# Kernel optimization log

Hardware: AMD Instinct MI355X
Metric: run time of the kernel (lower is better)

## Reference

```python
import jax, jax.numpy as jnp
import numpy as np

B, T, N, F = 32, 64, 128, 128
U, K1, K2 = 64, 64, 32
EPS = 1e-3  # keras BatchNormalization default epsilon
SLOPE = 0.01  # LeakyReLU negative_slope


def setup_inputs() -> dict:
    key = jax.random.key(0)
    ks = jax.random.split(key, 16)
    g = lambda k, sh, s=0.05: jax.random.normal(k, sh, dtype=jnp.float32) * s
    inp = {
        "x": jax.random.normal(ks[0], (B, T, F), dtype=jnp.float32),
        "a": jax.random.uniform(ks[1], (B, N, N), dtype=jnp.float32),
        # LSTM (keras gate order i, f, c, o)
        "lstm_k": g(ks[2], (F, 4 * U)),
        "lstm_r": g(ks[3], (U, 4 * U)),
        "lstm_b": jnp.zeros((4 * U,), jnp.float32),
        # BatchNorm params (inference form: gamma, beta, moving mean, moving var)
        "bnl_g": jnp.ones((U,), jnp.float32), "bnl_b": jnp.zeros((U,), jnp.float32),
        "bnl_m": jnp.zeros((U,), jnp.float32), "bnl_v": jnp.ones((U,), jnp.float32),
        "w1": g(ks[4], (U, K1)), "b1": jnp.zeros((K1,), jnp.float32),
        "bn1_g": jnp.ones((K1,), jnp.float32), "bn1_b": jnp.zeros((K1,), jnp.float32),
        "bn1_m": jnp.zeros((K1,), jnp.float32), "bn1_v": jnp.ones((K1,), jnp.float32),
        "w2": g(ks[5], (K1, K2)), "b2": jnp.zeros((K2,), jnp.float32),
        "bn2_g": jnp.ones((K2,), jnp.float32), "bn2_b": jnp.zeros((K2,), jnp.float32),
        "bn2_m": jnp.zeros((K2,), jnp.float32), "bn2_v": jnp.ones((K2,), jnp.float32),
        "d1_w": g(ks[6], (T * N * K2, 3), 0.01), "d1_b": jnp.zeros((3,), jnp.float32),
        "d2_w": g(ks[7], (3, N)), "d2_b": jnp.zeros((N,), jnp.float32),
    }
    return inp


def _bn(x, g, b, m, v):
    return (x - m) * (g * jax.lax.rsqrt(v + EPS)) + b


def _leaky(x):
    return jnp.where(x >= 0, x, SLOPE * x)


def _lstm(x, Wk, Wr, b):
    # x: [B, T, F] -> hs: [B, T, U]
    xz = jnp.einsum('btf,fg->btg', x, Wk) + b  # precompute input projections
    u = Wr.shape[0]
    h0 = jnp.zeros((x.shape[0], u), x.dtype)
    c0 = jnp.zeros((x.shape[0], u), x.dtype)

    def step(carry, zt):
        h, c = carry
        z = zt + h @ Wr
        i, f, g_, o = jnp.split(z, 4, axis=-1)
        i = jax.nn.sigmoid(i); f = jax.nn.sigmoid(f)
        g_ = jnp.tanh(g_); o = jax.nn.sigmoid(o)
        c = f * c + i * g_
        h = o * jnp.tanh(c)
        return (h, c), h

    _, hs = jax.lax.scan(step, (h0, c0), xz.transpose(1, 0, 2))
    return hs.transpose(1, 0, 2)


def reference(x, a, lstm_k, lstm_r, lstm_b, bnl_g, bnl_b, bnl_m, bnl_v,
              w1, b1, bn1_g, bn1_b, bn1_m, bn1_v,
              w2, b2, bn2_g, bn2_b, bn2_m, bn2_v,
              d1_w, d1_b, d2_w, d2_b):
    h = _lstm(x, lstm_k, lstm_r, lstm_b)              # [B, T, U]
    h = _bn(h, bnl_g, bnl_b, bnl_m, bnl_v)            # inference BN; dropout is identity
    # tile each timestep's LSTM output over the N nodes, then GCN1
    support1 = jnp.einsum('btu,uk->btk', h, w1)       # [B, T, K1] (identical across nodes)
    sup1 = jnp.broadcast_to(support1[:, :, None, :], (h.shape[0], h.shape[1], N, w1.shape[1]))
    g1 = jnp.einsum('bij,btjk->btik', a, sup1) + b1   # adjacency matmul
    g1 = _leaky(g1)
    g1 = _bn(g1, bn1_g, bn1_b, bn1_m, bn1_v)
    # GCN2
    sup2 = jnp.einsum('btnk,km->btnm', g1, w2)
    g2 = jnp.einsum('bij,btjm->btim', a, sup2) + b2
    g2 = _leaky(g2)
    g2 = _bn(g2, bn2_g, bn2_b, bn2_m, bn2_v)          # [B, T, N, K2]
    flat = g2.reshape(g2.shape[0], -1)                # [B, T*N*K2]
    d1 = jax.nn.relu(flat @ d1_w + d1_b)              # [B, 3]
    return d1 @ d2_w + d2_b                           # [B, N]
```

## Files before the change

kernel.cpp:

```cpp
#include <hip/hip_runtime.h>

#define BB 32
#define TT 64
#define NN 128
#define FF 128
#define UU 64
#define K1 64
#define K2 32
#define G4 256
#define EPSV 1e-3f
#define SLOPE 0.01f

#define ALD 136
#define SLD 136
#define WLD 72

typedef __attribute__((ext_vector_type(8))) short short8;
typedef __attribute__((ext_vector_type(4))) float f32x4;

__device__ __forceinline__ float sigmoidf_(float x) {
  return __builtin_amdgcn_rcpf(1.f + __expf(-x));
}
__device__ __forceinline__ float tanhf_(float x) {
  return 1.f - 2.f * __builtin_amdgcn_rcpf(__expf(2.f * x) + 1.f);
}
__device__ __forceinline__ float leaky_(float x) { return x >= 0.f ? x : SLOPE * x; }
__device__ __forceinline__ unsigned short f2bf(float x) {
  union { float f; unsigned u; } v; v.f = x;
  unsigned r = v.u + 0x7fff + ((v.u >> 16) & 1);
  return (unsigned short)(r >> 16);
}

__global__ __launch_bounds__(256) void k_pre(const float* __restrict__ x,
                                             const float* __restrict__ wk,
                                             const float* __restrict__ bias,
                                             const float* __restrict__ a,
                                             const float* __restrict__ w2,
                                             float* __restrict__ xz,
                                             float* __restrict__ rsum,
                                             unsigned short* __restrict__ apad,
                                             unsigned short* __restrict__ w2t) {
  int tid = threadIdx.x;
  if (blockIdx.x < 32) {
    int b = blockIdx.x;
    int wave = tid >> 6, lane = tid & 63;
    const float* ab = a + (size_t)b * NN * NN;
    for (int r = 0; r < 32; ++r) {
      int row = wave * 32 + r;
      float2 v = *(const float2*)(ab + (size_t)row * NN + lane * 2);
      float s = v.x + v.y;
#pragma unroll
      for (int off = 32; off >= 1; off >>= 1) s += __shfl_down(s, off);
      if (lane == 0) rsum[b * NN + row] = s;
    }
    unsigned short* ap = apad + (size_t)b * NN * ALD;
    for (int idx = tid; idx < NN * NN; idx += 256) {
      int i = idx >> 7, j = idx & 127;
      ap[i * ALD + j] = f2bf(ab[idx]);
    }
    if (b == 0) {
      for (int idx = tid; idx < K1 * K2; idx += 256) {
        int k = idx >> 5, m = idx & 31;
        w2t[m * WLD + k] = f2bf(w2[idx]);
      }
    }
  } else {
    __shared__ float xs[8][FF];
    int row0 = (blockIdx.x - 32) * 8;
    for (int i = tid; i < 8 * FF; i += 256) xs[i >> 7][i & 127] = x[(size_t)row0 * FF + i];
    __syncthreads();
    int g = tid;
    float acc[8];
    float bg = bias[g];
#pragma unroll
    for (int r = 0; r < 8; ++r) acc[r] = bg;
    for (int f = 0; f < FF; ++f) {
      float w = wk[f * G4 + g];
#pragma unroll
      for (int r = 0; r < 8; ++r) acc[r] += xs[r][f] * w;
    }
#pragma unroll
    for (int r = 0; r < 8; ++r) xz[(size_t)(row0 + r) * G4 + g] = acc[r];
  }
}

__global__ __launch_bounds__(256, 1) void k_lstm(const float* __restrict__ xz,
                                                 const float* __restrict__ wr,
                                                 const float* __restrict__ bnl_g,
                                                 const float* __restrict__ bnl_b,
                                                 const float* __restrict__ bnl_m,
                                                 const float* __restrict__ bnl_v,
                                                 float* __restrict__ hbn) {
  __shared__ __align__(16) float hsh[2][UU];
  __shared__ __align__(16) float hist[TT][UU];
  int tid = threadIdx.x;
  int wave = tid >> 6;
  int lane = tid & 63;
  int q = lane >> 4, up = lane & 15;
  int u = wave * 16 + up;
  int g = q * 64 + u;
  int b = blockIdx.x;

  float wcol[UU];
#pragma unroll
  for (int v = 0; v < UU; ++v) wcol[v] = wr[v * G4 + g];

  float bscale = bnl_g[u] * rsqrtf(bnl_v[u] + EPSV);
  float boff = bnl_b[u] - bnl_m[u] * bscale;

  if (tid < UU) hsh[0][tid] = 0.f;

  const float* xzb = xz + (size_t)b * TT * G4;
  float cur = xzb[g];
  float c = 0.f;

  for (int t = 0; t < TT; ++t) {
    __syncthreads();
    float nxt = (t + 1 < TT) ? xzb[(t + 1) * G4 + g] : 0.f;
    const float4* h4 = (const float4*)hsh[t & 1];
    float acc0 = cur, acc1 = 0.f, acc2 = 0.f, acc3 = 0.f;
#pragma unroll
    for (int p = 0; p < 16; p += 4) {
      float4 v0 = h4[p], v1 = h4[p + 1], v2 = h4[p + 2], v3 = h4[p + 3];
      acc0 += v0.x * wcol[4 * p + 0] + v0.y * wcol[4 * p + 1] + v0.z * wcol[4 * p + 2] + v0.w * wcol[4 * p + 3];
      acc1 += v1.x * wcol[4 * p + 4] + v1.y * wcol[4 * p + 5] + v1.z * wcol[4 * p + 6] + v1.w * wcol[4 * p + 7];
      acc2 += v2.x * wcol[4 * p + 8] + v2.y * wcol[4 * p + 9] + v2.z * wcol[4 * p + 10] + v2.w * wcol[4 * p + 11];
      acc3 += v3.x * wcol[4 * p + 12] + v3.y * wcol[4 * p + 13] + v3.z * wcol[4 * p + 14] + v3.w * wcol[4 * p + 15];
    }
    float z = (acc0 + acc1) + (acc2 + acc3);
    float zi = __shfl(z, up);
    float zf = __shfl(z, up + 16);
    float zg = __shfl(z, up + 32);
    float zo = __shfl(z, up + 48);
    float i_ = sigmoidf_(zi), f_ = sigmoidf_(zf), g_ = tanhf_(zg), o_ = sigmoidf_(zo);
    c = f_ * c + i_ * g_;
    float h = o_ * tanhf_(c);
    if (q == 0) {
      hsh[(t & 1) ^ 1][u] = h;
      hist[t][u] = h * bscale + boff;
    }
    cur = nxt;
  }
  __syncthreads();
  const float4* hs4 = (const float4*)&hist[0][0];
  float4* hb4 = (float4*)(hbn + (size_t)b * TT * UU);
#pragma unroll
  for (int k = 0; k < 4; ++k) hb4[tid + k * 256] = hs4[tid + k * 256];
}

__global__ __launch_bounds__(256) void k_gcn(
    const float* __restrict__ hbn, const float* __restrict__ w1,
    const float* __restrict__ rsum,
    const unsigned short* __restrict__ apad, const unsigned short* __restrict__ w2t,
    const float* __restrict__ b1,
    const float* __restrict__ bn1_g, const float* __restrict__ bn1_b,
    const float* __restrict__ bn1_m, const float* __restrict__ bn1_v,
    const float* __restrict__ b2,
    const float* __restrict__ bn2_g, const float* __restrict__ bn2_b,
    const float* __restrict__ bn2_m, const float* __restrict__ bn2_v,
    const float* __restrict__ d1w, float* __restrict__ part) {
  __shared__ unsigned short a_lds[NN * ALD];
  __shared__ unsigned short s2_lds[K2 * SLD];
  __shared__ unsigned short w2_lds[K2 * WLD];
  __shared__ float4 gp[K1];
  __shared__ float r_lds[NN];
  __shared__ float p2[3 * K2];
  __shared__ float red[12];

  int blk = blockIdx.x;
  int b = blk & 31, t = blk >> 5;
  int tid = threadIdx.x;
  int lane = tid & 63, wave = tid >> 6;
  int l15 = lane & 15, l4 = lane >> 4;

  {
    const uint4* src = (const uint4*)(apad + (size_t)b * NN * ALD);
    uint4* dst = (uint4*)a_lds;
    for (int i = tid; i < NN * ALD / 8; i += 256) dst[i] = src[i];
  }
  {
    const uint2* src = (const uint2*)w2t;
    uint2* dst = (uint2*)w2_lds;
    for (int i = tid; i < K2 * WLD / 4; i += 256) dst[i] = src[i];
  }
  if (tid < K1) {
    float hv = hbn[((size_t)b * TT + t) * UU + tid];
    float s1v = 0.f;
#pragma unroll
    for (int u = 0; u < UU; ++u) s1v += __shfl(hv, u) * w1[u * K1 + tid];
    float s = bn1_g[tid] * rsqrtf(bn1_v[tid] + EPSV);
    gp[tid] = make_float4(s1v, b1[tid], s, bn1_b[tid] - bn1_m[tid] * s);
  }
  if (tid >= 64 && tid < 64 + NN) r_lds[tid - 64] = rsum[b * NN + (tid - 64)];
  if (tid >= 192 && tid < 192 + K2) {
    int m = tid - 192;
    float s = bn2_g[m] * rsqrtf(bn2_v[m] + EPSV);
    p2[m] = b2[m];
    p2[K2 + m] = s;
    p2[2 * K2 + m] = bn2_b[m] - bn2_m[m] * s;
  }
  __syncthreads();

  f32x4 z4 = {0.f, 0.f, 0.f, 0.f};

  {
    float rj0 = r_lds[(wave * 2 + 0) * 16 + l15];
    float rj1 = r_lds[(wave * 2 + 1) * 16 + l15];
    f32x4 acc[2][2];
    acc[0][0] = z4; acc[0][1] = z4; acc[1][0] = z4; acc[1][1] = z4;
#pragma unroll
    for (int kt = 0; kt < 2; ++kt) {
      float4 gpv[8];
#pragma unroll
      for (int e = 0; e < 8; ++e) gpv[e] = gp[kt * 32 + l4 * 8 + e];
      short8 bfrag0 = *((const short8*)&w2_lds[(0 + l15) * WLD + kt * 32 + l4 * 8]);
      short8 bfrag1 = *((const short8*)&w2_lds[(16 + l15) * WLD + kt * 32 + l4 * 8]);
#pragma unroll
      for (int jt = 0; jt < 2; ++jt) {
        float rj = jt ? rj1 : rj0;
        short8 af;
#pragma unroll
        for (int e = 0; e < 8; ++e) {
          float4 p = gpv[e];
          float v = leaky_(rj * p.x + p.y) * p.z + p.w;
          af[e] = (short)f2bf(v);
        }
        acc[jt][0] = __builtin_amdgcn_mfma_f32_16x16x32_bf16(af, bfrag0, acc[jt][0], 0, 0, 0);
        acc[jt][1] = __builtin_amdgcn_mfma_f32_16x16x32_bf16(af, bfrag1, acc[jt][1], 0, 0, 0);
      }
    }
#pragma unroll
    for (int jt = 0; jt < 2; ++jt) {
      int jbase = (wave * 2 + jt) * 16 + l4 * 4;
#pragma unroll
      for (int mt = 0; mt < 2; ++mt) {
        int m = mt * 16 + l15;
        unsigned lo = (unsigned)f2bf(acc[jt][mt][0]) | ((unsigned)f2bf(acc[jt][mt][1]) << 16);
        unsigned hi = (unsigned)f2bf(acc[jt][mt][2]) | ((unsigned)f2bf(acc[jt][mt][3]) << 16);
        uint2 val; val.x = lo; val.y = hi;
        *((uint2*)&s2_lds[m * SLD + jbase]) = val;
      }
    }
  }
  __syncthreads();

  float c0 = 0.f, c1 = 0.f, c2 = 0.f;
  {
    f32x4 acc[2][2];
    acc[0][0] = z4; acc[0][1] = z4; acc[1][0] = z4; acc[1][1] = z4;
#pragma unroll
    for (int kt = 0; kt < 4; ++kt) {
      short8 bfrag0 = *((const short8*)&s2_lds[(0 + l15) * SLD + kt * 32 + l4 * 8]);
      short8 bfrag1 = *((const short8*)&s2_lds[(16 + l15) * SLD + kt * 32 + l4 * 8]);
#pragma unroll
      for (int it = 0; it < 2; ++it) {
        int i = (wave * 2 + it) * 16 + l15;
        short8 afrag = *((const short8*)&a_lds[i * ALD + kt * 32 + l4 * 8]);
        acc[it][0] = __builtin_amdgcn_mfma_f32_16x16x32_bf16(afrag, bfrag0, acc[it][0], 0, 0, 0);
        acc[it][1] = __builtin_amdgcn_mfma_f32_16x16x32_bf16(afrag, bfrag1, acc[it][1], 0, 0, 0);
      }
    }
    const float* dw = d1w + (size_t)t * NN * K2 * 3;
#pragma unroll
    for (int it = 0; it < 2; ++it) {
      int ibase = (wave * 2 + it) * 16 + l4 * 4;
#pragma unroll
      for (int mt = 0; mt < 2; ++mt) {
        int m = mt * 16 + l15;
        float bb = p2[m], bs = p2[K2 + m], bo = p2[2 * K2 + m];
#pragma unroll
        for (int r = 0; r < 4; ++r) {
          int i = ibase + r;
          float g2 = leaky_(acc[it][mt][r] + bb) * bs + bo;
          const float* dp = dw + ((size_t)i * K2 + m) * 3;
          c0 += g2 * dp[0];
          c1 += g2 * dp[1];
          c2 += g2 * dp[2];
        }
      }
    }
  }
#pragma unroll
  for (int off = 32; off >= 1; off >>= 1) {
    c0 += __shfl_down(c0, off);
    c1 += __shfl_down(c1, off);
    c2 += __shfl_down(c2, off);
  }
  if (lane == 0) { red[wave * 3 + 0] = c0; red[wave * 3 + 1] = c1; red[wave * 3 + 2] = c2; }
  __syncthreads();
  if (tid == 0) {
    float s0 = 0.f, s1v = 0.f, s2v = 0.f;
    for (int w = 0; w < 4; ++w) { s0 += red[w * 3]; s1v += red[w * 3 + 1]; s2v += red[w * 3 + 2]; }
    part[((size_t)b * TT + t) * 3 + 0] = s0;
    part[((size_t)b * TT + t) * 3 + 1] = s1v;
    part[((size_t)b * TT + t) * 3 + 2] = s2v;
  }
}

__global__ __launch_bounds__(128) void k_out(const float* __restrict__ part,
                                             const float* __restrict__ d1b,
                                             const float* __restrict__ d2w,
                                             const float* __restrict__ d2b,
                                             float* __restrict__ out) {
  int b = blockIdx.x, n = threadIdx.x;
  float s[3] = {0.f, 0.f, 0.f};
  const float* p = part + (size_t)b * TT * 3;
  for (int t = 0; t < TT; ++t) {
    s[0] += p[t * 3];
    s[1] += p[t * 3 + 1];
    s[2] += p[t * 3 + 2];
  }
  float o = d2b[n];
#pragma unroll
  for (int c = 0; c < 3; ++c) {
    float d = s[c] + d1b[c];
    d = d > 0.f ? d : 0.f;
    o += d * d2w[c * NN + n];
  }
  out[b * NN + n] = o;
}

extern "C" void kernel_launch(void* const* d_in, const int* in_sizes, int n_in,
                              void* d_out, int out_size, void* d_ws, size_t ws_size,
                              hipStream_t stream) {
  const float* x      = (const float*)d_in[0];
  const float* a      = (const float*)d_in[1];
  const float* lstm_k = (const float*)d_in[2];
  const float* lstm_r = (const float*)d_in[3];
  const float* lstm_b = (const float*)d_in[4];
  const float* bnl_g  = (const float*)d_in[5];
  const float* bnl_b  = (const float*)d_in[6];
  const float* bnl_m  = (const float*)d_in[7];
  const float* bnl_v  = (const float*)d_in[8];
  const float* w1     = (const float*)d_in[9];
  const float* b1     = (const float*)d_in[10];
  const float* bn1_g  = (const float*)d_in[11];
  const float* bn1_b  = (const float*)d_in[12];
  const float* bn1_m  = (const float*)d_in[13];
  const float* bn1_v  = (const float*)d_in[14];
  const float* w2     = (const float*)d_in[15];
  const float* b2     = (const float*)d_in[16];
  const float* bn2_g  = (const float*)d_in[17];
  const float* bn2_b  = (const float*)d_in[18];
  const float* bn2_m  = (const float*)d_in[19];
  const float* bn2_v  = (const float*)d_in[20];
  const float* d1_w   = (const float*)d_in[21];
  const float* d1_b   = (const float*)d_in[22];
  const float* d2_w   = (const float*)d_in[23];
  const float* d2_b   = (const float*)d_in[24];
  float* out = (float*)d_out;

  char* ws = (char*)d_ws;
  float* xz            = (float*)(ws + 0);
  float* hbn           = (float*)(ws + 2097152);
  float* rsum          = (float*)(ws + 2621440);
  float* part          = (float*)(ws + 2637824);
  unsigned short* apad = (unsigned short*)(ws + 2662400);
  unsigned short* w2t  = (unsigned short*)(ws + 3776512);

  k_pre<<<32 + BB * TT / 8, 256, 0, stream>>>(x, lstm_k, lstm_b, a, w2, xz, rsum, apad, w2t);
  k_lstm<<<BB, 256, 0, stream>>>(xz, lstm_r, bnl_g, bnl_b, bnl_m, bnl_v, hbn);
  k_gcn<<<BB * TT, 256, 0, stream>>>(hbn, w1, rsum, apad, w2t, b1, bn1_g, bn1_b, bn1_m, bn1_v,
                                     b2, bn2_g, bn2_b, bn2_m, bn2_v, d1_w, part);
  k_out<<<BB, 128, 0, stream>>>(part, d1_b, d2_w, d2_b, out);
}
```

Baseline: 85.89 us.

## Preload LSTM inputs to LDS, transpose recurrent weights, coalesce dense-weight reads

The LSTM kernel now reads a pre-transposed recurrent weight matrix with float4 loads and stages the whole per-batch input projection in LDS up front, so the recurrence no longer issues global loads on each step. In the GCN kernel the second-layer result is written through LDS so each thread can read a contiguous slice of the dense-layer weights with float4 loads, replacing strided 3-float scalar reads. The cost is extra LDS traffic and two more block barriers in the GCN kernel, plus a larger LDS footprint in the LSTM kernel.

After: 100.8 us. +17.4%, slower.

```diff
diff --git a/kernel.cpp b/kernel.cpp
--- a/kernel.cpp
+++ b/kernel.cpp
@@ -36,10 +36,12 @@
                                              const float* __restrict__ bias,
                                              const float* __restrict__ a,
                                              const float* __restrict__ w2,
+                                             const float* __restrict__ wr,
                                              float* __restrict__ xz,
                                              float* __restrict__ rsum,
                                              unsigned short* __restrict__ apad,
-                                             unsigned short* __restrict__ w2t) {
+                                             unsigned short* __restrict__ w2t,
+                                             float* __restrict__ wrt) {
   int tid = threadIdx.x;
   if (blockIdx.x < 32) {
     int b = blockIdx.x;
@@ -64,6 +66,12 @@
         w2t[m * WLD + k] = f2bf(w2[idx]);
       }
     }
+    if (b == 1) {
+      for (int idx = tid; idx < G4 * UU; idx += 256) {
+        int gg = idx >> 6, v = idx & 63;
+        wrt[idx] = wr[v * G4 + gg];
+      }
+    }
   } else {
     __shared__ float xs[8][FF];
     int row0 = (blockIdx.x - 32) * 8;
@@ -85,14 +93,15 @@
 }
 
 __global__ __launch_bounds__(256, 1) void k_lstm(const float* __restrict__ xz,
-                                                 const float* __restrict__ wr,
+                                                 const float* __restrict__ wrt,
                                                  const float* __restrict__ bnl_g,
                                                  const float* __restrict__ bnl_b,
                                                  const float* __restrict__ bnl_m,
                                                  const float* __restrict__ bnl_v,
                                                  float* __restrict__ hbn) {
+  __shared__ __align__(16) float xz_lds[TT * G4];
+  __shared__ __align__(16) float hist[TT][UU];
   __shared__ __align__(16) float hsh[2][UU];
-  __shared__ __align__(16) float hist[TT][UU];
   int tid = threadIdx.x;
   int wave = tid >> 6;
   int lane = tid & 63;
@@ -102,23 +111,26 @@
   int b = blockIdx.x;
 
   float wcol[UU];
-#pragma unroll
-  for (int v = 0; v < UU; ++v) wcol[v] = wr[v * G4 + g];
-
+  {
+    const float4* wp = (const float4*)(wrt + (size_t)g * UU);
+#pragma unroll
+    for (int k = 0; k < 16; ++k) ((float4*)wcol)[k] = wp[k];
+  }
+  {
+    const float4* src = (const float4*)(xz + (size_t)b * TT * G4);
+    float4* dst = (float4*)xz_lds;
+#pragma unroll
+    for (int k = 0; k < 16; ++k) dst[tid + k * 256] = src[tid + k * 256];
+  }
   float bscale = bnl_g[u] * rsqrtf(bnl_v[u] + EPSV);
   float boff = bnl_b[u] - bnl_m[u] * bscale;
-
   if (tid < UU) hsh[0][tid] = 0.f;
-
-  const float* xzb = xz + (size_t)b * TT * G4;
-  float cur = xzb[g];
   float c = 0.f;
+  __syncthreads();
 
   for (int t = 0; t < TT; ++t) {
-    __syncthreads();
-    float nxt = (t + 1 < TT) ? xzb[(t + 1) * G4 + g] : 0.f;
     const float4* h4 = (const float4*)hsh[t & 1];
-    float acc0 = cur, acc1 = 0.f, acc2 = 0.f, acc3 = 0.f;
+    float acc0 = xz_lds[t * G4 + g], acc1 = 0.f, acc2 = 0.f, acc3 = 0.f;
 #pragma unroll
     for (int p = 0; p < 16; p += 4) {
       float4 v0 = h4[p], v1 = h4[p + 1], v2 = h4[p + 2], v3 = h4[p + 3];
@@ -139,9 +151,8 @@
       hsh[(t & 1) ^ 1][u] = h;
       hist[t][u] = h * bscale + boff;
     }
-    cur = nxt;
-  }
-  __syncthreads();
+    __syncthreads();
+  }
   const float4* hs4 = (const float4*)&hist[0][0];
   float4* hb4 = (float4*)(hbn + (size_t)b * TT * UU);
 #pragma unroll
@@ -159,7 +170,7 @@
     const float* __restrict__ bn2_g, const float* __restrict__ bn2_b,
     const float* __restrict__ bn2_m, const float* __restrict__ bn2_v,
     const float* __restrict__ d1w, float* __restrict__ part) {
-  __shared__ unsigned short a_lds[NN * ALD];
+  __shared__ __align__(16) unsigned short a_lds[NN * ALD];
   __shared__ unsigned short s2_lds[K2 * SLD];
   __shared__ unsigned short w2_lds[K2 * WLD];
   __shared__ float4 gp[K1];
@@ -244,40 +255,55 @@
   }
   __syncthreads();
 
+  f32x4 acc[2][2];
+  acc[0][0] = z4; acc[0][1] = z4; acc[1][0] = z4; acc[1][1] = z4;
+#pragma unroll
+  for (int kt = 0; kt < 4; ++kt) {
+    short8 bfrag0 = *((const short8*)&s2_lds[(0 + l15) * SLD + kt * 32 + l4 * 8]);
+    short8 bfrag1 = *((const short8*)&s2_lds[(16 + l15) * SLD + kt * 32 + l4 * 8]);
+#pragma unroll
+    for (int it = 0; it < 2; ++it) {
+      int i = (wave * 2 + it) * 16 + l15;
+      short8 afrag = *((const short8*)&a_lds[i * ALD + kt * 32 + l4 * 8]);
+      acc[it][0] = __builtin_amdgcn_mfma_f32_16x16x32_bf16(afrag, bfrag0, acc[it][0], 0, 0, 0);
+      acc[it][1] = __builtin_amdgcn_mfma_f32_16x16x32_bf16(afrag, bfrag1, acc[it][1], 0, 0, 0);
+    }
+  }
+  __syncthreads();
+
+  float* g2l = (float*)a_lds;
+#pragma unroll
+  for (int it = 0; it < 2; ++it) {
+    int ibase = (wave * 2 + it) * 16 + l4 * 4;
+#pragma unroll
+    for (int mt = 0; mt < 2; ++mt) {
+      int m = mt * 16 + l15;
+      float bb = p2[m], bs = p2[K2 + m], bo = p2[2 * K2 + m];
+#pragma unroll
+      for (int r = 0; r < 4; ++r) {
+        g2l[(ibase + r) * 33 + m] = leaky_(acc[it][mt][r] + bb) * bs + bo;
+      }
+    }
+  }
+  __syncthreads();
+
   float c0 = 0.f, c1 = 0.f, c2 = 0.f;
   {
-    f32x4 acc[2][2];
-    acc[0][0] = z4; acc[0][1] = z4; acc[1][0] = z4; acc[1][1] = z4;
-#pragma unroll
-    for (int kt = 0; kt < 4; ++kt) {
-      short8 bfrag0 = *((const short8*)&s2_lds[(0 + l15) * SLD + kt * 32 + l4 * 8]);
-      short8 bfrag1 = *((const short8*)&s2_lds[(16 + l15) * SLD + kt * 32 + l4 * 8]);
-#pragma unroll
-      for (int it = 0; it < 2; ++it) {
-        int i = (wave * 2 + it) * 16 + l15;
-        short8 afrag = *((const short8*)&a_lds[i * ALD + kt * 32 + l4 * 8]);
-        acc[it][0] = __builtin_amdgcn_mfma_f32_16x16x32_bf16(afrag, bfrag0, acc[it][0], 0, 0, 0);
-        acc[it][1] = __builtin_amdgcn_mfma_f32_16x16x32_bf16(afrag, bfrag1, acc[it][1], 0, 0, 0);
-      }
-    }
-    const float* dw = d1w + (size_t)t * NN * K2 * 3;
-#pragma unroll
-    for (int it = 0; it < 2; ++it) {
-      int ibase = (wave * 2 + it) * 16 + l4 * 4;
-#pragma unroll
-      for (int mt = 0; mt < 2; ++mt) {
-        int m = mt * 16 + l15;
-        float bb = p2[m], bs = p2[K2 + m], bo = p2[2 * K2 + m];
-#pragma unroll
-        for (int r = 0; r < 4; ++r) {
-          int i = ibase + r;
-          float g2 = leaky_(acc[it][mt][r] + bb) * bs + bo;
-          const float* dp = dw + ((size_t)i * K2 + m) * 3;
-          c0 += g2 * dp[0];
-          c1 += g2 * dp[1];
-          c2 += g2 * dp[2];
-        }
-      }
+    const float4* dw4 = (const float4*)(d1w + (size_t)t * (NN * K2 * 3)) + tid * 12;
+    float w[48];
+#pragma unroll
+    for (int j = 0; j < 12; ++j) {
+      float4 v = dw4[j];
+      w[4 * j + 0] = v.x; w[4 * j + 1] = v.y; w[4 * j + 2] = v.z; w[4 * j + 3] = v.w;
+    }
+    int L0 = tid * 16;
+#pragma unroll
+    for (int k = 0; k < 16; ++k) {
+      int L = L0 + k;
+      float g2 = g2l[(L >> 5) * 33 + (L & 31)];
+      c0 += g2 * w[3 * k + 0];
+      c1 += g2 * w[3 * k + 1];
+      c2 += g2 * w[3 * k + 2];
     }
   }
 #pragma unroll
@@ -357,9 +383,11 @@
   float* part          = (float*)(ws + 2637824);
   unsigned short* apad = (unsigned short*)(ws + 2662400);
   unsigned short* w2t  = (unsigned short*)(ws + 3776512);
-
-  k_pre<<<32 + BB * TT / 8, 256, 0, stream>>>(x, lstm_k, lstm_b, a, w2, xz, rsum, apad, w2t);
-  k_lstm<<<BB, 256, 0, stream>>>(xz, lstm_r, bnl_g, bnl_b, bnl_m, bnl_v, hbn);
+  float* wrt           = (float*)(ws + 3781120);
+
+  k_pre<<<32 + BB * TT / 8, 256, 0, stream>>>(x, lstm_k, lstm_b, a, w2, lstm_r,
+                                              xz, rsum, apad, w2t, wrt);
+  k_lstm<<<BB, 256, 0, stream>>>(xz, wrt, bnl_g, bnl_b, bnl_m, bnl_v, hbn);
   k_gcn<<<BB * TT, 256, 0, stream>>>(hbn, w1, rsum, apad, w2t, b1, bn1_g, bn1_b, bn1_m, bn1_v,
                                      b2, bn2_g, bn2_b, bn2_m, bn2_v, d1_w, part);
   k_out<<<BB, 128, 0, stream>>>(part, d1_b, d2_w, d2_b, out);
```

## Run LSTM recurrence in a single wave with packed fp16 dot products

Applied to the files above, without the earlier changes.

The LSTM kernel now uses one 64-lane wave per batch row, with each lane computing all four gates for one hidden unit. This removes the per-step block barrier and the cross-lane shuffles. Recurrent weights are pre-packed as fp16 pairs in the preprocessing kernel and applied with fdot2, halving the multiply-add count. The input projections for the whole sequence are staged in LDS first. The trade-offs are reduced precision of the recurrent matmul, 64 KB of LDS per block, and a serial chain that still depends on one wave's latency.

Measured after the change: 80.31 us. 1.07x faster.

```diff
diff --git a/kernel.cpp b/kernel.cpp
--- a/kernel.cpp
+++ b/kernel.cpp
@@ -17,6 +17,7 @@
 
 typedef __attribute__((ext_vector_type(8))) short short8;
 typedef __attribute__((ext_vector_type(4))) float f32x4;
+typedef __attribute__((ext_vector_type(2))) __fp16 half2v;
 
 __device__ __forceinline__ float sigmoidf_(float x) {
   return __builtin_amdgcn_rcpf(1.f + __expf(-x));
@@ -36,10 +37,12 @@
                                              const float* __restrict__ bias,
                                              const float* __restrict__ a,
                                              const float* __restrict__ w2,
+                                             const float* __restrict__ wr,
                                              float* __restrict__ xz,
                                              float* __restrict__ rsum,
                                              unsigned short* __restrict__ apad,
-                                             unsigned short* __restrict__ w2t) {
+                                             unsigned short* __restrict__ w2t,
+                                             unsigned* __restrict__ wrp) {
   int tid = threadIdx.x;
   if (blockIdx.x < 32) {
     int b = blockIdx.x;
@@ -64,6 +67,18 @@
         w2t[m * WLD + k] = f2bf(w2[idx]);
       }
     }
+    if (b == 1) {
+      for (int idx = tid; idx < 4 * 32 * UU; idx += 256) {
+        int u2 = idx & 63;
+        int p = (idx >> 6) & 31;
+        int gate = idx >> 11;
+        int col = gate * UU + u2;
+        union { __fp16 h[2]; unsigned u; } pk;
+        pk.h[0] = (__fp16)wr[(2 * p) * G4 + col];
+        pk.h[1] = (__fp16)wr[(2 * p + 1) * G4 + col];
+        wrp[idx] = pk.u;
+      }
+    }
   } else {
     __shared__ float xs[8][FF];
     int row0 = (blockIdx.x - 32) * 8;
@@ -84,68 +99,64 @@
   }
 }
 
-__global__ __launch_bounds__(256, 1) void k_lstm(const float* __restrict__ xz,
-                                                 const float* __restrict__ wr,
-                                                 const float* __restrict__ bnl_g,
-                                                 const float* __restrict__ bnl_b,
-                                                 const float* __restrict__ bnl_m,
-                                                 const float* __restrict__ bnl_v,
-                                                 float* __restrict__ hbn) {
-  __shared__ __align__(16) float hsh[2][UU];
-  __shared__ __align__(16) float hist[TT][UU];
-  int tid = threadIdx.x;
-  int wave = tid >> 6;
-  int lane = tid & 63;
-  int q = lane >> 4, up = lane & 15;
-  int u = wave * 16 + up;
-  int g = q * 64 + u;
+__global__ __launch_bounds__(64, 1) void k_lstm(const float* __restrict__ xz,
+                                                const unsigned* __restrict__ wrp,
+                                                const float* __restrict__ bnl_g,
+                                                const float* __restrict__ bnl_b,
+                                                const float* __restrict__ bnl_m,
+                                                const float* __restrict__ bnl_v,
+                                                float* __restrict__ hbn) {
+  __shared__ __align__(16) float xz_lds[TT * G4];
+  __shared__ __align__(16) __fp16 h16[UU];
+  int u = threadIdx.x;
   int b = blockIdx.x;
 
-  float wcol[UU];
-#pragma unroll
-  for (int v = 0; v < UU; ++v) wcol[v] = wr[v * G4 + g];
+  {
+    const float4* src = (const float4*)(xz + (size_t)b * TT * G4);
+    float4* dst = (float4*)xz_lds;
+#pragma unroll
+    for (int k = 0; k < 64; ++k) dst[u + k * 64] = src[u + k * 64];
+  }
+  unsigned wv[4][32];
+#pragma unroll
+  for (int gate = 0; gate < 4; ++gate)
+#pragma unroll
+    for (int p = 0; p < 32; ++p) wv[gate][p] = wrp[(gate * 32 + p) * UU + u];
 
   float bscale = bnl_g[u] * rsqrtf(bnl_v[u] + EPSV);
   float boff = bnl_b[u] - bnl_m[u] * bscale;
-
-  if (tid < UU) hsh[0][tid] = 0.f;
-
-  const float* xzb = xz + (size_t)b * TT * G4;
-  float cur = xzb[g];
+  h16[u] = (__fp16)0.f;
   float c = 0.f;
+  float* hb = hbn + (size_t)b * TT * UU;
 
   for (int t = 0; t < TT; ++t) {
-    __syncthreads();
-    float nxt = (t + 1 < TT) ? xzb[(t + 1) * G4 + g] : 0.f;
-    const float4* h4 = (const float4*)hsh[t & 1];
-    float acc0 = cur, acc1 = 0.f, acc2 = 0.f, acc3 = 0.f;
-#pragma unroll
-    for (int p = 0; p < 16; p += 4) {
-      float4 v0 = h4[p], v1 = h4[p + 1], v2 = h4[p + 2], v3 = h4[p + 3];
-      acc0 += v0.x * wcol[4 * p + 0] + v0.y * wcol[4 * p + 1] + v0.z * wcol[4 * p + 2] + v0.w * wcol[4 * p + 3];
-      acc1 += v1.x * wcol[4 * p + 4] + v1.y * wcol[4 * p + 5] + v1.z * wcol[4 * p + 6] + v1.w * wcol[4 * p + 7];
-      acc2 += v2.x * wcol[4 * p + 8] + v2.y * wcol[4 * p + 9] + v2.z * wcol[4 * p + 10] + v2.w * wcol[4 * p + 11];
-      acc3 += v3.x * wcol[4 * p + 12] + v3.y * wcol[4 * p + 13] + v3.z * wcol[4 * p + 14] + v3.w * wcol[4 * p + 15];
-    }
-    float z = (acc0 + acc1) + (acc2 + acc3);
-    float zi = __shfl(z, up);
-    float zf = __shfl(z, up + 16);
-    float zg = __shfl(z, up + 32);
-    float zo = __shfl(z, up + 48);
+    unsigned hw[32];
+    {
+      const uint4* hq = (const uint4*)h16;
+#pragma unroll
+      for (int k = 0; k < 8; ++k) {
+        uint4 v = hq[k];
+        hw[4 * k + 0] = v.x; hw[4 * k + 1] = v.y; hw[4 * k + 2] = v.z; hw[4 * k + 3] = v.w;
+      }
+    }
+    float zi = xz_lds[t * G4 + u];
+    float zf = xz_lds[t * G4 + 64 + u];
+    float zg = xz_lds[t * G4 + 128 + u];
+    float zo = xz_lds[t * G4 + 192 + u];
+#pragma unroll
+    for (int p = 0; p < 32; ++p) {
+      half2v hh = __builtin_bit_cast(half2v, hw[p]);
+      zi = __builtin_amdgcn_fdot2(__builtin_bit_cast(half2v, wv[0][p]), hh, zi, false);
+      zf = __builtin_amdgcn_fdot2(__builtin_bit_cast(half2v, wv[1][p]), hh, zf, false);
+      zg = __builtin_amdgcn_fdot2(__builtin_bit_cast(half2v, wv[2][p]), hh, zg, false);
+      zo = __builtin_amdgcn_fdot2(__builtin_bit_cast(half2v, wv[3][p]), hh, zo, false);
+    }
     float i_ = sigmoidf_(zi), f_ = sigmoidf_(zf), g_ = tanhf_(zg), o_ = sigmoidf_(zo);
     c = f_ * c + i_ * g_;
     float h = o_ * tanhf_(c);
-    if (q == 0) {
-      hsh[(t & 1) ^ 1][u] = h;
-      hist[t][u] = h * bscale + boff;
-    }
-    cur = nxt;
-  }
-  __syncthreads();
-  const float4* hs4 = (const float4*)&hist[0][0];
-  float4* hb4 = (float4*)(hbn + (size_t)b * TT * UU);
-#pragma unroll
-  for (int k = 0; k < 4; ++k) hb4[tid + k * 256] = hs4[tid + k * 256];
+    h16[u] = (__fp16)h;
+    hb[t * UU + u] = h * bscale + boff;
+  }
 }
 
 __global__ __launch_bounds__(256) void k_gcn(
@@ -357,9 +368,11 @@
   float* part          = (float*)(ws + 2637824);
   unsigned short* apad = (unsigned short*)(ws + 2662400);
   unsigned short* w2t  = (unsigned short*)(ws + 3776512);
-
-  k_pre<<<32 + BB * TT / 8, 256, 0, stream>>>(x, lstm_k, lstm_b, a, w2, xz, rsum, apad, w2t);
-  k_lstm<<<BB, 256, 0, stream>>>(xz, lstm_r, bnl_g, bnl_b, bnl_m, bnl_v, hbn);
+  unsigned* wrp        = (unsigned*)(ws + 3781120);
+
+  k_pre<<<32 + BB * TT / 8, 256, 0, stream>>>(x, lstm_k, lstm_b, a, w2, lstm_r,
+                                              xz, rsum, apad, w2t, wrp);
+  k_lstm<<<BB, 64, 0, stream>>>(xz, wrp, bnl_g, bnl_b, bnl_m, bnl_v, hbn);
   k_gcn<<<BB * TT, 256, 0, stream>>>(hbn, w1, rsum, apad, w2t, b1, bn1_g, bn1_b, bn1_m, bn1_v,
                                      b2, bn2_g, bn2_b, bn2_m, bn2_v, d1_w, part);
   k_out<<<BB, 128, 0, stream>>>(part, d1_b, d2_w, d2_b, out);
```
